# Optimization experiments

Hardware: AMD Instinct MI355X
Metric: run time of the kernel (lower is better)

## Reference

```python
import jax, jax.numpy as jnp
import numpy as np

N, D = 50000, 1000
FH1, FH2 = 256, 128
GH1, GH2, H = 64, 30, 3
NC = 10
E = 800000
BN_EPS = 1e-5


def setup_inputs() -> dict:
    key = jax.random.key(0)
    ks = iter(jax.random.split(key, 48))
    nk = lambda: next(ks)
    r = lambda *s: jax.random.normal(nk(), s, jnp.float32) * 0.05
    g = lambda n: 1.0 + jax.random.normal(nk(), (n,), jnp.float32) * 0.01
    return dict(
        x=jax.random.normal(nk(), (N, D), jnp.float32),
        edge_index=jax.random.randint(nk(), (2, E), 0, N, dtype=jnp.int32),
        enc_w1=r(D, FH1), enc_b1=r(FH1), enc_g1=g(FH1), enc_bt1=r(FH1),
        enc_w2=r(FH1, FH2), enc_b2=r(FH2), enc_g2=g(FH2), enc_bt2=r(FH2),
        gat1_w=r(FH2, H * GH1), gat1_asrc=r(H, GH1), gat1_adst=r(H, GH1), gat1_b=r(H * GH1),
        gat2_w=r(H * GH1, GH2), gat2_asrc=r(1, GH2), gat2_adst=r(1, GH2), gat2_b=r(GH2),
        gat3_w=r(H * GH1, GH2), gat3_asrc=r(1, GH2), gat3_adst=r(1, GH2), gat3_b=r(GH2),
        dec_w1=r(GH2, FH2), dec_b1=r(FH2), dec_g1=g(FH2), dec_bt1=r(FH2),
        dec_w2=r(FH2, FH1), dec_b2=r(FH1), dec_g2=g(FH1), dec_bt2=r(FH1),
        dec_w3=r(FH1, D), dec_b3=r(D),
        clu_w1=r(GH2, FH2), clu_b1=r(FH2), clu_g1=g(FH2), clu_bt1=r(FH2),
        clu_w2=r(FH2, NC), clu_b2=r(NC),
    )


def _bn_elu(h, w, b, gm, bt):
    # Linear -> BatchNorm1d (batch stats) -> ELU; dropout is identity at eval
    h = h @ w + b
    m = h.mean(0)
    v = h.var(0)
    return jax.nn.elu(gm * (h - m) * jax.lax.rsqrt(v + BN_EPS) + bt)


def _gat(h, src, dst, n, w, a_src, a_dst, b, heads, oc, concat):
    # PyG GATConv: per-head linear, edge-wise LeakyReLU(0.2) scores,
    # softmax over incoming edges of each dst node, weighted scatter-sum.
    hh = (h @ w).reshape(n, heads, oc)            # [N,H,C]
    s_src = jnp.sum(hh * a_src, -1)               # [N,H]
    s_dst = jnp.sum(hh * a_dst, -1)               # [N,H]
    e = jax.nn.leaky_relu(s_src[src] + s_dst[dst], negative_slope=0.2)  # [E,H]
    m = jax.ops.segment_max(e, dst, num_segments=n)
    p = jnp.exp(e - m[dst])
    denom = jax.ops.segment_sum(p, dst, num_segments=n)
    alpha = p / denom[dst]                        # [E,H]
    msg = hh[src] * alpha[..., None]              # [E,H,C]
    out = jax.ops.segment_sum(msg, dst, num_segments=n)
    out = out.reshape(n, heads * oc) if concat else out.mean(1)
    return out + b


def reference(x, edge_index,
              enc_w1, enc_b1, enc_g1, enc_bt1, enc_w2, enc_b2, enc_g2, enc_bt2,
              gat1_w, gat1_asrc, gat1_adst, gat1_b,
              gat2_w, gat2_asrc, gat2_adst, gat2_b,
              gat3_w, gat3_asrc, gat3_adst, gat3_b,
              dec_w1, dec_b1, dec_g1, dec_bt1, dec_w2, dec_b2, dec_g2, dec_bt2, dec_w3, dec_b3,
              clu_w1, clu_b1, clu_g1, clu_bt1, clu_w2, clu_b2):
    n = x.shape[0]
    loops = jnp.arange(n, dtype=edge_index.dtype)  # GATConv add_self_loops=True
    src = jnp.concatenate([edge_index[0], loops])
    dst = jnp.concatenate([edge_index[1], loops])

    h = _bn_elu(x, enc_w1, enc_b1, enc_g1, enc_bt1)
    h = _bn_elu(h, enc_w2, enc_b2, enc_g2, enc_bt2)
    h = jax.nn.relu(_gat(h, src, dst, n, gat1_w, gat1_asrc, gat1_adst, gat1_b, H, GH1, True))
    mu = _gat(h, src, dst, n, gat2_w, gat2_asrc, gat2_adst, gat2_b, 1, GH2, False)
    logvar = _gat(h, src, dst, n, gat3_w, gat3_asrc, gat3_adst, gat3_b, 1, GH2, False)
    z = mu  # eval-mode reparameterize returns mu

    d = _bn_elu(z, dec_w1, dec_b1, dec_g1, dec_bt1)
    d = _bn_elu(d, dec_w2, dec_b2, dec_g2, dec_bt2)
    x_rec = d @ dec_w3 + dec_b3

    c = _bn_elu(z, clu_w1, clu_b1, clu_g1, clu_bt1)
    pred = jax.nn.softmax(c @ clu_w2 + clu_b2, axis=1)
    return (pred, x_rec, z, mu, logvar)
```

## Files before the change

kernel.cpp:

```cpp
#include <hip/hip_runtime.h>
#include <hip/hip_bf16.h>

typedef short short8 __attribute__((ext_vector_type(8)));
typedef short short4v __attribute__((ext_vector_type(4)));
typedef float f32x4 __attribute__((ext_vector_type(4)));

static __device__ __forceinline__ short f2bf(float f){
  __hip_bfloat16 h = __float2bfloat16(f);
  return __builtin_bit_cast(short, h);
}
static __device__ __forceinline__ float b2f(short s){
  unsigned int u = ((unsigned int)(unsigned short)s) << 16;
  return __builtin_bit_cast(float, u);
}
static __device__ __forceinline__ float lrelu(float x){ return x > 0.f ? x : 0.2f*x; }
static __device__ __forceinline__ float eluf(float x){ return x > 0.f ? x : (__expf(x)-1.f); }
static __device__ __forceinline__ int imin(int a,int b){ return a<b?a:b; }

typedef const __attribute__((address_space(1))) void as1_void;
typedef __attribute__((address_space(3))) void as3_void;
static __device__ __forceinline__ void gload16(const void* g, void* l){
  __builtin_amdgcn_global_load_lds((as1_void*)g, (as3_void*)l, 16, 0, 0);
}
template<int NN> __device__ __forceinline__ void wait_vm(){
  if constexpr (NN==0) asm volatile("s_waitcnt vmcnt(0)" ::: "memory");
  else if constexpr (NN==3) asm volatile("s_waitcnt vmcnt(3)" ::: "memory");
  else if constexpr (NN==4) asm volatile("s_waitcnt vmcnt(4)" ::: "memory");
  else if constexpr (NN==6) asm volatile("s_waitcnt vmcnt(6)" ::: "memory");
  else if constexpr (NN==8) asm volatile("s_waitcnt vmcnt(8)" ::: "memory");
  else asm volatile("s_waitcnt vmcnt(0)" ::: "memory");
}

template<int BN, bool OBF16, bool CST, bool SMAX, bool G23S, bool G1S>
static __device__ __forceinline__ void gemm_core(int wg, short* lds,
    const short* __restrict__ A, int lda, const short* __restrict__ Bt, int ldb,
    void* __restrict__ Cv, int ldc, const float* __restrict__ bias,
    int M, int N, int K, int nbn,
    float* __restrict__ o_sum, float* __restrict__ o_sq,
    float* __restrict__ s2s, float* __restrict__ s2d,
    float* __restrict__ s3s, float* __restrict__ s3d,
    const float* __restrict__ a2s, const float* __restrict__ a2d,
    const float* __restrict__ a3s, const float* __restrict__ a3d)
{
  constexpr int BM = 128, BK = 32, GPR = 4;
  constexpr int WM = BM/2, WN = BN/2;
  constexpr int FM = WM/16, FN = WN/16;
  constexpr int AI = (BM*GPR)/(4*64);
  constexpr int BI_T = (BN*GPR)/64;
  constexpr bool BDUP = (BI_T < 4);
  constexpr int BI = BDUP ? BI_T : BI_T/4;
  constexpr int LPT = AI + BI;
  constexpr int TS = (BM+BN)*BK;

  const int tid = threadIdx.x, wid = tid>>6, lane = tid&63;
  const int wm = wid>>1, wn = wid&1;
  int bmt = wg / nbn, bnt = wg - bmt*nbn;
  const int bm = bmt*BM, bn = bnt*BN;
  const int lr = lane&15, lg = lane>>4;
  const int nt = (K + BK - 1)/BK;

  f32x4 acc[FM][FN] = {};

  auto STAGE = [&](int t){
    int buf = t % 3, k0 = t*BK;
    #pragma unroll
    for (int i=0;i<AI;i++){
      int ci = wid*AI + i;
      int c = ci*64 + lane;
      int row = c>>2, g = c&3;
      int gr = imin(bm+row, M-1);
      const short* src = A + (size_t)gr*lda + k0 + ((g ^ (row&3))<<3);
      gload16(src, &lds[buf*TS + ci*512]);
    }
    #pragma unroll
    for (int i=0;i<BI;i++){
      int bi = BDUP ? i : wid*BI + i;
      int c = bi*64 + lane;
      int row = c>>2, g = c&3;
      const short* src = Bt + (size_t)(bn+row)*ldb + k0 + ((g ^ (row&3))<<3);
      gload16(src, &lds[buf*TS + BM*BK + bi*512]);
    }
  };

  for (int s=0; s<2 && s<nt; ++s) STAGE(s);

  for (int t=0; t<nt; ++t){
    int newer = imin(nt, t+2) - t - 1;
    if (newer >= 1) wait_vm<LPT>();
    else wait_vm<0>();
    __builtin_amdgcn_s_barrier();
    __builtin_amdgcn_sched_barrier(0);
    if (t+2 < nt) STAGE(t+2);
    int buf = t % 3;
    short8 af[FM], bf[FN];
    #pragma unroll
    for (int m=0;m<FM;m++){
      int r = wm*WM + m*16 + lr;
      af[m] = *(short8*)&lds[buf*TS + r*BK + ((lg ^ (r&3))<<3)];
    }
    #pragma unroll
    for (int n=0;n<FN;n++){
      int r = wn*WN + n*16 + lr;
      bf[n] = *(short8*)&lds[buf*TS + BM*BK + r*BK + ((lg ^ (r&3))<<3)];
    }
    #pragma unroll
    for (int m=0;m<FM;m++)
      #pragma unroll
      for (int n=0;n<FN;n++)
        acc[m][n] = __builtin_amdgcn_mfma_f32_16x16x32_bf16(af[m], bf[n], acc[m][n], 0, 0, 0);
  }

  if (SMAX){
    #pragma unroll
    for (int m=0;m<FM;m++)
      #pragma unroll
      for (int q=0;q<4;q++){
        int row = bm + wm*WM + m*16 + lg*4 + q;
        float v = (lr < 10) ? (acc[m][0][q] + bias[lr]) : -3e38f;
        float mx = v;
        #pragma unroll
        for (int d=1; d<16; d<<=1) mx = fmaxf(mx, __shfl_xor(mx, d));
        float e = (lr < 10) ? __expf(v - mx) : 0.f;
        float sm = e;
        #pragma unroll
        for (int d=1; d<16; d<<=1) sm += __shfl_xor(sm, d);
        if (wn == 0 && lr < 10 && row < M)
          ((float*)Cv)[(size_t)row*10 + lr] = e/sm;
      }
    return;
  }

  #pragma unroll
  for (int m=0;m<FM;m++)
    #pragma unroll
    for (int n=0;n<FN;n++)
      #pragma unroll
      for (int q=0;q<4;q++){
        int row = bm + wm*WM + m*16 + lg*4 + q;
        int col = bn + wn*WN + n*16 + lr;
        if (row < M && col < N){
          float v = acc[m][n][q];
          if (bias) v += bias[col];
          if (OBF16) ((short*)Cv)[(size_t)row*ldc + col] = f2bf(v);
          else       ((float*)Cv)[(size_t)row*ldc + col] = v;
        }
      }

  if (G1S){
    int h = bnt;
    float a_s[FN], a_d[FN];
    #pragma unroll
    for (int n=0;n<FN;n++){
      int cl = wn*WN + n*16 + lr;
      a_s[n] = a2s[h*64 + cl];
      a_d[n] = a2d[h*64 + cl];
    }
    #pragma unroll
    for (int m=0;m<FM;m++)
      #pragma unroll
      for (int q=0;q<4;q++){
        int row = bm + wm*WM + m*16 + lg*4 + q;
        float ps = 0.f, pd = 0.f;
        #pragma unroll
        for (int n=0;n<FN;n++){ ps += acc[m][n][q]*a_s[n]; pd += acc[m][n][q]*a_d[n]; }
        #pragma unroll
        for (int d=1; d<16; d<<=1){ ps += __shfl_xor(ps, d); pd += __shfl_xor(pd, d); }
        if (lr == 0 && row < M){
          atomicAdd(&s2s[row*3+h], ps);
          atomicAdd(&s2d[row*3+h], pd);
        }
      }
  }

  if (G23S){
    float a_s[FN], a_d[FN];
    #pragma unroll
    for (int n=0;n<FN;n++){
      int cl = n*16 + lr;
      bool valid = cl < 30;
      a_s[n] = valid ? (wn ? a3s[cl] : a2s[cl]) : 0.f;
      a_d[n] = valid ? (wn ? a3d[cl] : a2d[cl]) : 0.f;
    }
    #pragma unroll
    for (int m=0;m<FM;m++)
      #pragma unroll
      for (int q=0;q<4;q++){
        int row = bm + wm*WM + m*16 + lg*4 + q;
        float ps = 0.f, pd = 0.f;
        #pragma unroll
        for (int n=0;n<FN;n++){ ps += acc[m][n][q]*a_s[n]; pd += acc[m][n][q]*a_d[n]; }
        #pragma unroll
        for (int d=1; d<16; d<<=1){ ps += __shfl_xor(ps, d); pd += __shfl_xor(pd, d); }
        if (lr == 0 && row < M){
          if (wn){ s3s[row] = ps; s3d[row] = pd; }
          else   { s2s[row] = ps; s2d[row] = pd; }
        }
      }
  }

  if (CST){
    #pragma unroll
    for (int n=0;n<FN;n++){
      float s = 0.f, q2 = 0.f;
      #pragma unroll
      for (int m=0;m<FM;m++)
        #pragma unroll
        for (int q=0;q<4;q++){
          int row = bm + wm*WM + m*16 + lg*4 + q;
          if (row < M){ float v = acc[m][n][q]; s += v; q2 += v*v; }
        }
      s  += __shfl_xor(s, 16);  s += __shfl_xor(s, 32);
      q2 += __shfl_xor(q2, 16); q2 += __shfl_xor(q2, 32);
      if (lg == 0){
        int col = bn + wn*WN + n*16 + lr;
        if (col < N){ atomicAdd(&o_sum[col], s); atomicAdd(&o_sq[col], q2); }
      }
    }
  }
}

static __device__ __forceinline__ int xcd_swz(int bid, int nwg){
  int q8 = nwg >> 3, r8 = nwg & 7;
  int xcd = bid & 7, pos = bid >> 3;
  return (xcd < r8 ? xcd*(q8+1) : r8*(q8+1) + (xcd-r8)*q8) + pos;
}

template<int BN, bool OBF16, bool CST, bool SMAX, bool G23S, bool G1S>
__global__ __launch_bounds__(256) void gemm_g(
    const short* __restrict__ A, int lda, const short* __restrict__ Bt, int ldb,
    void* __restrict__ Cv, int ldc, const float* __restrict__ bias,
    int M, int N, int K, int nbn,
    float* __restrict__ o_sum, float* __restrict__ o_sq,
    float* __restrict__ s2s, float* __restrict__ s2d,
    float* __restrict__ s3s, float* __restrict__ s3d,
    const float* __restrict__ a2s, const float* __restrict__ a2d,
    const float* __restrict__ a3s, const float* __restrict__ a3d)
{
  __shared__ short lds[3*(128+BN)*32];
  int wg = xcd_swz(blockIdx.x, gridDim.x);
  gemm_core<BN,OBF16,CST,SMAX,G23S,G1S>(wg, lds, A, lda, Bt, ldb, Cv, ldc, bias,
      M, N, K, nbn, o_sum, o_sq, s2s, s2d, s3s, s3d, a2s, a2d, a3s, a3d);
}

__global__ __launch_bounds__(256) void gemm_dual(
    const short* __restrict__ A1, int lda1, const short* __restrict__ B1, int ldb1,
    void* __restrict__ C1, int ldc1, const float* __restrict__ bias1, int N1, int K1,
    const short* __restrict__ A2, int lda2, const short* __restrict__ B2, int ldb2,
    void* __restrict__ C2, const float* __restrict__ bias2, int N2, int K2,
    int M, int split)
{
  __shared__ short lds[3*(128+128)*32];
  int wg = xcd_swz(blockIdx.x, gridDim.x);
  if (wg < split){
    gemm_core<128,false,false,false,false,false>(wg, lds, A1, lda1, B1, ldb1, C1, ldc1, bias1,
        M, N1, K1, 8, nullptr,nullptr, nullptr,nullptr,nullptr,nullptr, nullptr,nullptr,nullptr,nullptr);
  } else {
    gemm_core<32,false,false,true,false,false>(wg - split, lds, A2, lda2, B2, ldb2, C2, 10, bias2,
        M, N2, K2, 1, nullptr,nullptr, nullptr,nullptr,nullptr,nullptr, nullptr,nullptr,nullptr,nullptr);
  }
}

__global__ __launch_bounds__(256) void cvt_hist(const float* __restrict__ x, short* __restrict__ xb, int M,
                                                int CB, const int* __restrict__ d, int E, int* __restrict__ deg){
  int b = blockIdx.x;
  if (b < CB){
    int row = b*2 + (threadIdx.x>>7);
    int c8  = (threadIdx.x&127)*8;
    if (row >= M || c8 >= 1000) return;
    const float* p = x + (size_t)row*1000 + c8;
    float4 f0 = *(const float4*)p, f1 = *(const float4*)(p+4);
    short8 o;
    o[0]=f2bf(f0.x);o[1]=f2bf(f0.y);o[2]=f2bf(f0.z);o[3]=f2bf(f0.w);
    o[4]=f2bf(f1.x);o[5]=f2bf(f1.y);o[6]=f2bf(f1.z);o[7]=f2bf(f1.w);
    *(short8*)&xb[(size_t)row*1000 + c8] = o;
  } else {
    int i = (b - CB)*256 + threadIdx.x;
    if (i < E) atomicAdd(&deg[d[i]], 1);
  }
}

struct WEnt { const float* src; short* dst; int K, N, KP, NR; };
struct WTab { WEnt e[10]; };
__global__ __launch_bounds__(256) void wtrans_all(WTab tab){
  WEnt w = tab.e[blockIdx.y];
  int gid = blockIdx.x*256 + threadIdx.x;
  if (gid >= w.NR * w.KP) return;
  int n = gid / w.KP, k = gid - n*w.KP;
  float v = (k < w.K && n < w.N) ? w.src[(size_t)k*w.N + n] : 0.f;
  w.dst[gid] = f2bf(v);
}

template<int C>
__global__ __launch_bounds__(256) void bn_elu_apply2(const short* __restrict__ H, short* __restrict__ O,
    int M, float invM,
    const float* __restrict__ ssum, const float* __restrict__ ssq,
    const float* __restrict__ g, const float* __restrict__ bt){
  __shared__ float sc[C], sh[C];
  for (int c = threadIdx.x; c < C; c += 256){
    float mn  = ssum[c]*invM;
    float var = ssq[c]*invM - mn*mn;
    float s = g[c]*rsqrtf(var + 1e-5f);
    sc[c] = s; sh[c] = bt[c] - mn*s;
  }
  __syncthreads();
  int total8 = M*(C/8);
  for (int i = blockIdx.x*256+threadIdx.x; i < total8; i += gridDim.x*256){
    short8 v = ((const short8*)H)[i];
    int cb = (i*8) & (C-1);
    short8 o;
    #pragma unroll
    for (int j=0;j<8;j++) o[j] = f2bf(eluf(b2f(v[j])*sc[cb+j]+sh[cb+j]));
    ((short8*)O)[i] = o;
  }
}

__global__ __launch_bounds__(256) void bn_elu_split(const short* __restrict__ H,
    short* __restrict__ Od, short* __restrict__ Oc, int M, float invM,
    const float* __restrict__ ssum, const float* __restrict__ ssq,
    const float* __restrict__ gd, const float* __restrict__ btd,
    const float* __restrict__ gc, const float* __restrict__ btc){
  __shared__ float sc[256], sh[256];
  {
    int c = threadIdx.x;
    float mn  = ssum[c]*invM;
    float var = ssq[c]*invM - mn*mn;
    float gg = (c<128) ? gd[c] : gc[c-128];
    float bb = (c<128) ? btd[c] : btc[c-128];
    float s = gg*rsqrtf(var + 1e-5f);
    sc[c] = s; sh[c] = bb - mn*s;
  }
  __syncthreads();
  int total8 = M*32;
  for (int i = blockIdx.x*256+threadIdx.x; i < total8; i += gridDim.x*256){
    short8 v = ((const short8*)H)[i];
    int cb = (i*8) & 255;
    short8 o;
    #pragma unroll
    for (int j=0;j<8;j++) o[j] = f2bf(eluf(b2f(v[j])*sc[cb+j]+sh[cb+j]));
    int row = i>>5;
    short* O = (cb < 128) ? Od : Oc;
    *(short8*)&O[(size_t)row*128 + (cb&127)] = o;
  }
}

__global__ __launch_bounds__(256) void scan1(const int* __restrict__ deg, int* __restrict__ offs,
                                             int* __restrict__ bsum, int n){
  __shared__ int sm[256];
  int tid = threadIdx.x;
  int base = blockIdx.x*1024 + tid*4;
  int v0 = base+0<n ? deg[base+0] : 0;
  int v1 = base+1<n ? deg[base+1] : 0;
  int v2 = base+2<n ? deg[base+2] : 0;
  int v3 = base+3<n ? deg[base+3] : 0;
  int ts = v0+v1+v2+v3;
  sm[tid] = ts;
  __syncthreads();
  #pragma unroll
  for (int d=1; d<256; d<<=1){
    int t = (tid>=d) ? sm[tid-d] : 0;
    __syncthreads();
    sm[tid] += t;
    __syncthreads();
  }
  int ex = sm[tid] - ts;
  if (base+0<n) offs[base+0] = ex;
  if (base+1<n) offs[base+1] = ex+v0;
  if (base+2<n) offs[base+2] = ex+v0+v1;
  if (base+3<n) offs[base+3] = ex+v0+v1+v2;
  if (tid==255) bsum[blockIdx.x] = sm[255];
}
__global__ __launch_bounds__(256) void scan3(int* __restrict__ offs, const int* __restrict__ bsum,
                      int* __restrict__ cursor, int n, int total){
  __shared__ int base_sm;
  int tgt = blockIdx.x >> 2;
  if (threadIdx.x < 64){
    int j = threadIdx.x;
    int v = (j < tgt) ? bsum[j] : 0;
    #pragma unroll
    for (int d=32; d; d>>=1) v += __shfl_xor(v, d);
    if (j == 0) base_sm = v;
  }
  __syncthreads();
  int i = blockIdx.x*256 + threadIdx.x;
  if (i < n){ int v = offs[i] + base_sm; offs[i]=v; cursor[i]=v; }
  if (i == 0) offs[n] = total;
}
__global__ void scatter_kernel(const int* __restrict__ s, const int* __restrict__ d, int E,
                               int* __restrict__ cursor, int* __restrict__ csr){
  int i = blockIdx.x*256 + threadIdx.x;
  if (i < E){ int pos = atomicAdd(&cursor[d[i]], 1); csr[pos] = s[i]; }
}

__global__ __launch_bounds__(256) void gat1_gather_bf(const int* __restrict__ offs, const int* __restrict__ csr,
    const short* __restrict__ hh, const float* __restrict__ ss, const float* __restrict__ sd,
    const float* __restrict__ bias, short* __restrict__ out, int n){
  int w = threadIdx.x >> 6, lane = threadIdx.x & 63;
  int dst = blockIdx.x*4 + w;
  if (dst >= n) return;
  float sd0 = sd[dst*3+0], sd1 = sd[dst*3+1], sd2 = sd[dst*3+2];
  float p0 = __expf(lrelu(ss[dst*3+0]+sd0));
  float p1 = __expf(lrelu(ss[dst*3+1]+sd1));
  float p2 = __expf(lrelu(ss[dst*3+2]+sd2));
  const short* hr = hh + (size_t)dst*192;
  float a0 = p0*b2f(hr[lane]), a1 = p1*b2f(hr[64+lane]), a2 = p2*b2f(hr[128+lane]);
  float d0 = p0, d1 = p1, d2 = p2;
  int p = offs[dst], pe = offs[dst+1];
  int n0=0,n1=0,n2=0,n3=0;
  if (p+4 <= pe){ n0=csr[p]; n1=csr[p+1]; n2=csr[p+2]; n3=csr[p+3]; }
  while (p+4 <= pe){
    int s0=n0, s1=n1, s2=n2, s3=n3;
    int pn = p+4;
    if (pn+4 <= pe){ n0=csr[pn]; n1=csr[pn+1]; n2=csr[pn+2]; n3=csr[pn+3]; }
    float e00=ss[s0*3+0], e01=ss[s0*3+1], e02=ss[s0*3+2];
    float e10=ss[s1*3+0], e11=ss[s1*3+1], e12=ss[s1*3+2];
    float e20=ss[s2*3+0], e21=ss[s2*3+1], e22=ss[s2*3+2];
    float e30=ss[s3*3+0], e31=ss[s3*3+1], e32=ss[s3*3+2];
    const short* r0 = hh + (size_t)s0*192;
    const short* r1 = hh + (size_t)s1*192;
    const short* r2 = hh + (size_t)s2*192;
    const short* r3 = hh + (size_t)s3*192;
    float v00=b2f(r0[lane]), v01=b2f(r0[64+lane]), v02=b2f(r0[128+lane]);
    float v10=b2f(r1[lane]), v11=b2f(r1[64+lane]), v12=b2f(r1[128+lane]);
    float v20=b2f(r2[lane]), v21=b2f(r2[64+lane]), v22=b2f(r2[128+lane]);
    float v30=b2f(r3[lane]), v31=b2f(r3[64+lane]), v32=b2f(r3[128+lane]);
    float q00=__expf(lrelu(e00+sd0)), q01=__expf(lrelu(e01+sd1)), q02=__expf(lrelu(e02+sd2));
    float q10=__expf(lrelu(e10+sd0)), q11=__expf(lrelu(e11+sd1)), q12=__expf(lrelu(e12+sd2));
    float q20=__expf(lrelu(e20+sd0)), q21=__expf(lrelu(e21+sd1)), q22=__expf(lrelu(e22+sd2));
    float q30=__expf(lrelu(e30+sd0)), q31=__expf(lrelu(e31+sd1)), q32=__expf(lrelu(e32+sd2));
    a0 += q00*v00 + q10*v10 + q20*v20 + q30*v30;
    a1 += q01*v01 + q11*v11 + q21*v21 + q31*v31;
    a2 += q02*v02 + q12*v12 + q22*v22 + q32*v32;
    d0 += q00+q10+q20+q30;
    d1 += q01+q11+q21+q31;
    d2 += q02+q12+q22+q32;
    p = pn;
  }
  for (; p < pe; ++p){
    int src = csr[p];
    float q0 = __expf(lrelu(ss[src*3+0]+sd0));
    float q1 = __expf(lrelu(ss[src*3+1]+sd1));
    float q2 = __expf(lrelu(ss[src*3+2]+sd2));
    const short* sr = hh + (size_t)src*192;
    a0 += q0*b2f(sr[lane]); a1 += q1*b2f(sr[64+lane]); a2 += q2*b2f(sr[128+lane]);
    d0 += q0; d1 += q1; d2 += q2;
  }
  float v0 = a0/d0 + bias[lane];
  float v1 = a1/d1 + bias[64+lane];
  float v2 = a2/d2 + bias[128+lane];
  short* orow = out + (size_t)dst*192;
  orow[lane]      = f2bf(v0 > 0.f ? v0 : 0.f);
  orow[64+lane]   = f2bf(v1 > 0.f ? v1 : 0.f);
  orow[128+lane]  = f2bf(v2 > 0.f ? v2 : 0.f);
}

__global__ __launch_bounds__(256) void gat23_gather(const int* __restrict__ offs, const int* __restrict__ csr,
    const short* __restrict__ hh23,
    const float* __restrict__ s2s, const float* __restrict__ s2d,
    const float* __restrict__ s3s, const float* __restrict__ s3d,
    const float* __restrict__ b2, const float* __restrict__ b3,
    float* __restrict__ zs, float* __restrict__ mus, float* __restrict__ lvs,
    short* __restrict__ zbf, int n){
  int w = threadIdx.x >> 6, lane = threadIdx.x & 63;
  int dst = blockIdx.x*4 + w;
  if (dst >= n) return;
  bool lo = lane < 32;
  int c = lane & 31;
  bool valid = c < 30;
  float sdA = s2d[dst], sdB = s3d[dst];
  float sdx = lo ? sdA : sdB;
  const float* ssx = lo ? s2s : s3s;
  float p2 = __expf(lrelu(s2s[dst]+sdA));
  float p3 = __expf(lrelu(s3s[dst]+sdB));
  float val = valid ? b2f(hh23[(size_t)dst*64+lane]) : 0.f;
  float acc = (lo ? p2 : p3) * val;
  float den2 = p2, den3 = p3;
  int p = offs[dst], pe = offs[dst+1];
  int n0=0,n1=0,n2=0,n3=0;
  if (p+4 <= pe){ n0=csr[p]; n1=csr[p+1]; n2=csr[p+2]; n3=csr[p+3]; }
  while (p+4 <= pe){
    int s0=n0, s1=n1, s2i=n2, s3i=n3;
    int pn = p+4;
    if (pn+4 <= pe){ n0=csr[pn]; n1=csr[pn+1]; n2=csr[pn+2]; n3=csr[pn+3]; }
    float eA0=ssx[s0], eA1=ssx[s1], eA2=ssx[s2i], eA3=ssx[s3i];
    float f20=s2s[s0], f21=s2s[s1], f22=s2s[s2i], f23=s2s[s3i];
    float f30=s3s[s0], f31=s3s[s1], f32=s3s[s2i], f33=s3s[s3i];
    float v0 = valid ? b2f(hh23[(size_t)s0*64+lane]) : 0.f;
    float v1 = valid ? b2f(hh23[(size_t)s1*64+lane]) : 0.f;
    float v2 = valid ? b2f(hh23[(size_t)s2i*64+lane]) : 0.f;
    float v3 = valid ? b2f(hh23[(size_t)s3i*64+lane]) : 0.f;
    float qx0=__expf(lrelu(eA0+sdx)), qx1=__expf(lrelu(eA1+sdx));
    float qx2=__expf(lrelu(eA2+sdx)), qx3=__expf(lrelu(eA3+sdx));
    acc += qx0*v0 + qx1*v1 + qx2*v2 + qx3*v3;
    den2 += __expf(lrelu(f20+sdA)) + __expf(lrelu(f21+sdA)) + __expf(lrelu(f22+sdA)) + __expf(lrelu(f23+sdA));
    den3 += __expf(lrelu(f30+sdB)) + __expf(lrelu(f31+sdB)) + __expf(lrelu(f32+sdB)) + __expf(lrelu(f33+sdB));
    p = pn;
  }
  for (; p < pe; ++p){
    int src = csr[p];
    float q2 = __expf(lrelu(s2s[src]+sdA));
    float q3 = __expf(lrelu(s3s[src]+sdB));
    float v = valid ? b2f(hh23[(size_t)src*64+lane]) : 0.f;
    acc += (lo ? q2 : q3) * v;
    den2 += q2; den3 += q3;
  }
  if (lo){
    if (valid){
      float v = acc/den2 + b2[c];
      zs[(size_t)dst*30+c]  = v;
      mus[(size_t)dst*30+c] = v;
      zbf[(size_t)dst*32+c] = f2bf(v);
    } else {
      zbf[(size_t)dst*32+c] = 0;
    }
  } else if (valid){
    lvs[(size_t)dst*30+c] = acc/den3 + b3[c];
  }
}

static inline int cdiv(int a, int b){ return (a + b - 1) / b; }

extern "C" void kernel_launch(void* const* d_in, const int* in_sizes, int n_in,
                              void* d_out, int out_size, void* d_ws, size_t ws_size,
                              hipStream_t stream)
{
  const float* x        = (const float*)d_in[0];
  const int*   ei       = (const int*)  d_in[1];
  const float* enc_w1   = (const float*)d_in[2];
  const float* enc_g1   = (const float*)d_in[4];
  const float* enc_bt1  = (const float*)d_in[5];
  const float* enc_w2   = (const float*)d_in[6];
  const float* enc_g2   = (const float*)d_in[8];
  const float* enc_bt2  = (const float*)d_in[9];
  const float* gat1_w   = (const float*)d_in[10];
  const float* gat1_as  = (const float*)d_in[11];
  const float* gat1_ad  = (const float*)d_in[12];
  const float* gat1_b   = (const float*)d_in[13];
  const float* gat2_w   = (const float*)d_in[14];
  const float* gat2_as  = (const float*)d_in[15];
  const float* gat2_ad  = (const float*)d_in[16];
  const float* gat2_b   = (const float*)d_in[17];
  const float* gat3_w   = (const float*)d_in[18];
  const float* gat3_as  = (const float*)d_in[19];
  const float* gat3_ad  = (const float*)d_in[20];
  const float* gat3_b   = (const float*)d_in[21];
  const float* dec_w1   = (const float*)d_in[22];
  const float* dec_g1   = (const float*)d_in[24];
  const float* dec_bt1  = (const float*)d_in[25];
  const float* dec_w2   = (const float*)d_in[26];
  const float* dec_g2   = (const float*)d_in[28];
  const float* dec_bt2  = (const float*)d_in[29];
  const float* dec_w3   = (const float*)d_in[30];
  const float* dec_b3   = (const float*)d_in[31];
  const float* clu_w1   = (const float*)d_in[32];
  const float* clu_g1   = (const float*)d_in[34];
  const float* clu_bt1  = (const float*)d_in[35];
  const float* clu_w2   = (const float*)d_in[36];
  const float* clu_b2   = (const float*)d_in[37];

  const int N = in_sizes[0] / 1000;
  const int E = in_sizes[1] / 2;
  const int* e_src = ei;
  const int* e_dst = ei + E;
  const float invN = 1.f/(float)N;

  float* out  = (float*)d_out;
  float* pred = out;
  float* xrec = out + (size_t)N*10;
  float* zs   = xrec + (size_t)N*1000;
  float* mus  = zs  + (size_t)N*30;
  float* lvs  = mus + (size_t)N*30;

  char* ws = (char*)d_ws;
  size_t off = 0;
  auto alloc = [&](size_t bytes)->char*{
    char* p = ws + off;
    off = (off + bytes + 255) & ~(size_t)255;
    return p;
  };
  short* t_enc1  = (short*)alloc(256*1024*2);
  short* t_enc2  = (short*)alloc(128*256*2);
  short* t_gat1  = (short*)alloc(256*128*2);
  short* t_gat23 = (short*)alloc(64*192*2);
  short* t_dc1   = (short*)alloc(256*32*2);
  short* t_dec2  = (short*)alloc(256*128*2);
  short* t_dec3  = (short*)alloc(1024*256*2);
  short* t_clu2  = (short*)alloc(32*128*2);
  float* h1f  = (float*)alloc((size_t)N*256*4);
  short* h1b  = (short*)alloc((size_t)N*256*2);
  float* h2f  = (float*)alloc((size_t)N*128*4);
  short* h2b  = (short*)alloc((size_t)N*128*2);
  short* hh1b = (short*)alloc((size_t)N*192*2);
  short* h3b  = (short*)alloc((size_t)N*192*2);
  float* hh23f= (float*)alloc((size_t)N*64*4);
  short* zbf  = (short*)alloc((size_t)N*32*2);
  size_t zcnt = 2048 + (size_t)6*N + (N+1);
  float* stats= (float*)alloc(zcnt*4);
  float* ss1  = stats + 2048;
  float* sd1  = ss1 + (size_t)3*N;
  int*   deg  = (int*)(sd1 + (size_t)3*N);
  float* s2s  = (float*)alloc((size_t)N*4);
  float* s2d  = (float*)alloc((size_t)N*4);
  float* s3s  = (float*)alloc((size_t)N*4);
  float* s3d  = (float*)alloc((size_t)N*4);
  int*   offs = (int*)alloc((size_t)(N+1)*4);
  int*   curp = (int*)alloc((size_t)(N+1)*4);
  int*   bsum = (int*)alloc(256*4);
  int*   csr  = (int*)alloc((size_t)E*4);
  short* xb     = h1b;
  short* h1pre  = (short*)h1f;
  short* h2pre  = (short*)h2f;
  short* hh23b  = (short*)hh23f;
  short* dc1pre = (short*)h2f;
  short* d1b    = h3b;
  short* c1b    = hh1b;
  short* d2pre  = (short*)h1f;
  short* d2b    = h1b;
  float* st_enc1 = stats, *st_enc2 = stats+512, *st_dc1 = stats+768, *st_dec2 = stats+1280;

  WTab tab;
  tab.e[0]  = {enc_w1, t_enc1, 1000, 256, 1024, 256};
  tab.e[1]  = {enc_w2, t_enc2, 256, 128, 256, 128};
  tab.e[2]  = {gat1_w, t_gat1, 128, 192, 128, 256};
  tab.e[3]  = {gat2_w, t_gat23, 192, 30, 192, 32};
  tab.e[4]  = {gat3_w, t_gat23 + 32*192, 192, 30, 192, 32};
  tab.e[5]  = {dec_w1, t_dc1, 30, 128, 32, 128};
  tab.e[6]  = {clu_w1, t_dc1 + 128*32, 30, 128, 32, 128};
  tab.e[7]  = {dec_w2, t_dec2, 128, 256, 128, 256};
  tab.e[8]  = {dec_w3, t_dec3, 256, 1000, 256, 1024};
  tab.e[9]  = {clu_w2, t_clu2, 128, 10, 128, 32};
  wtrans_all<<<dim3(1024, 10), 256, 0, stream>>>(tab);
  hipMemsetAsync(stats, 0, zcnt*4, stream);

  int CB = cdiv(N, 2);
  cvt_hist<<<CB + cdiv(E,256), 256, 0, stream>>>(x, xb, N, CB, e_dst, E, deg);

  int nb = cdiv(N, 1024);
  scan1<<<nb, 256, 0, stream>>>(deg, offs, bsum, N);
  scan3<<<cdiv(N,256), 256, 0, stream>>>(offs, bsum, curp, N, E);
  scatter_kernel<<<cdiv(E,256), 256, 0, stream>>>(e_src, e_dst, E, curp, csr);

  const int MB = cdiv(N, 128);

  gemm_g<128,true,true,false,false,false><<<MB*2, 256, 0, stream>>>(
      xb, 1000, t_enc1, 1024, h1pre, 256, nullptr, N, 256, 1000, 2,
      st_enc1, st_enc1+256, nullptr,nullptr,nullptr,nullptr, nullptr,nullptr,nullptr,nullptr);
  bn_elu_apply2<256><<<2048, 256, 0, stream>>>(h1pre, h1b, N, invN, st_enc1, st_enc1+256, enc_g1, enc_bt1);

  gemm_g<128,true,true,false,false,false><<<MB, 256, 0, stream>>>(
      h1b, 256, t_enc2, 256, h2pre, 128, nullptr, N, 128, 256, 1,
      st_enc2, st_enc2+128, nullptr,nullptr,nullptr,nullptr, nullptr,nullptr,nullptr,nullptr);
  bn_elu_apply2<128><<<2048, 256, 0, stream>>>(h2pre, h2b, N, invN, st_enc2, st_enc2+128, enc_g2, enc_bt2);

  gemm_g<64,true,false,false,false,true><<<MB*3, 256, 0, stream>>>(
      h2b, 128, t_gat1, 128, hh1b, 192, nullptr, N, 192, 128, 3,
      nullptr,nullptr, ss1,sd1,nullptr,nullptr, gat1_as,gat1_ad,nullptr,nullptr);
  gat1_gather_bf<<<cdiv(N,4), 256, 0, stream>>>(offs, csr, hh1b, ss1, sd1, gat1_b, h3b, N);

  gemm_g<64,true,false,false,true,false><<<MB, 256, 0, stream>>>(
      h3b, 192, t_gat23, 192, hh23b, 64, nullptr, N, 64, 192, 1,
      nullptr,nullptr, s2s,s2d,s3s,s3d, gat2_as,gat2_ad,gat3_as,gat3_ad);
  gat23_gather<<<cdiv(N,4), 256, 0, stream>>>(offs, csr, hh23b, s2s, s2d, s3s, s3d, gat2_b, gat3_b, zs, mus, lvs, zbf, N);

  gemm_g<128,true,true,false,false,false><<<MB*2, 256, 0, stream>>>(
      zbf, 32, t_dc1, 32, dc1pre, 256, nullptr, N, 256, 32, 2,
      st_dc1, st_dc1+256, nullptr,nullptr,nullptr,nullptr, nullptr,nullptr,nullptr,nullptr);
  bn_elu_split<<<2048, 256, 0, stream>>>(dc1pre, d1b, c1b, N, invN, st_dc1, st_dc1+256, dec_g1, dec_bt1, clu_g1, clu_bt1);

  gemm_g<128,true,true,false,false,false><<<MB*2, 256, 0, stream>>>(
      d1b, 128, t_dec2, 128, d2pre, 256, nullptr, N, 256, 128, 2,
      st_dec2, st_dec2+256, nullptr,nullptr,nullptr,nullptr, nullptr,nullptr,nullptr,nullptr);
  bn_elu_apply2<256><<<2048, 256, 0, stream>>>(d2pre, d2b, N, invN, st_dec2, st_dec2+256, dec_g2, dec_bt2);

  gemm_dual<<<MB*8 + MB, 256, 0, stream>>>(
      d2b, 256, t_dec3, 256, xrec, 1000, dec_b3, 1000, 256,
      c1b, 128, t_clu2, 128, pred, clu_b2, 10, 128,
      N, MB*8);
}
```

Baseline: 616.0 us.

## Fuse fp32-to-bf16 input conversion into the first encoder GEMM

```diff
diff --git a/kernel.cpp b/kernel.cpp
--- a/kernel.cpp
+++ b/kernel.cpp
@@ -29,6 +29,12 @@
   else if constexpr (NN==6) asm volatile("s_waitcnt vmcnt(6)" ::: "memory");
   else if constexpr (NN==8) asm volatile("s_waitcnt vmcnt(8)" ::: "memory");
   else asm volatile("s_waitcnt vmcnt(0)" ::: "memory");
+}
+
+static __device__ __forceinline__ int xcd_swz(int bid, int nwg){
+  int q8 = nwg >> 3, r8 = nwg & 7;
+  int xcd = bid & 7, pos = bid >> 3;
+  return (xcd < r8 ? xcd*(q8+1) : r8*(q8+1) + (xcd-r8)*q8) + pos;
 }
 
 template<int BN, bool OBF16, bool CST, bool SMAX, bool G23S, bool G1S>
@@ -219,12 +225,6 @@
   }
 }
 
-static __device__ __forceinline__ int xcd_swz(int bid, int nwg){
-  int q8 = nwg >> 3, r8 = nwg & 7;
-  int xcd = bid & 7, pos = bid >> 3;
-  return (xcd < r8 ? xcd*(q8+1) : r8*(q8+1) + (xcd-r8)*q8) + pos;
-}
-
 template<int BN, bool OBF16, bool CST, bool SMAX, bool G23S, bool G1S>
 __global__ __launch_bounds__(256) void gemm_g(
     const short* __restrict__ A, int lda, const short* __restrict__ Bt, int ldb,
@@ -260,23 +260,109 @@
   }
 }
 
-__global__ __launch_bounds__(256) void cvt_hist(const float* __restrict__ x, short* __restrict__ xb, int M,
-                                                int CB, const int* __restrict__ d, int E, int* __restrict__ deg){
-  int b = blockIdx.x;
-  if (b < CB){
-    int row = b*2 + (threadIdx.x>>7);
-    int c8  = (threadIdx.x&127)*8;
-    if (row >= M || c8 >= 1000) return;
-    const float* p = x + (size_t)row*1000 + c8;
-    float4 f0 = *(const float4*)p, f1 = *(const float4*)(p+4);
-    short8 o;
-    o[0]=f2bf(f0.x);o[1]=f2bf(f0.y);o[2]=f2bf(f0.z);o[3]=f2bf(f0.w);
-    o[4]=f2bf(f1.x);o[5]=f2bf(f1.y);o[6]=f2bf(f1.z);o[7]=f2bf(f1.w);
-    *(short8*)&xb[(size_t)row*1000 + c8] = o;
-  } else {
-    int i = (b - CB)*256 + threadIdx.x;
-    if (i < E) atomicAdd(&deg[d[i]], 1);
-  }
+__global__ __launch_bounds__(256) void gemm_f32a(
+    const float* __restrict__ A, int lda, const short* __restrict__ Bt, int ldb,
+    short* __restrict__ C, int ldc,
+    int M, int N, int K, int nbn,
+    float* __restrict__ o_sum, float* __restrict__ o_sq)
+{
+  constexpr int BM=128, BN=128, BK=32;
+  constexpr int ATS = BM*64;
+  constexpr int TSH = ATS + BN*32;
+  __shared__ short lds[3*TSH];
+  const int tid=threadIdx.x, wid=tid>>6, lane=tid&63;
+  const int wm=wid>>1, wn=wid&1;
+  int wg = xcd_swz(blockIdx.x, gridDim.x);
+  int bmt = wg/nbn, bnt = wg - bmt*nbn;
+  const int bm=bmt*BM, bn=bnt*BN;
+  const int lr=lane&15, lg=lane>>4;
+  const int nt=(K+BK-1)/BK;
+  f32x4 acc[4][4]={};
+
+  auto STAGE=[&](int t){
+    int buf=t%3, k0=t*BK;
+    #pragma unroll
+    for (int i=0;i<4;i++){
+      int ci = wid*4+i;
+      int c = ci*64+lane;
+      int row=c>>3, g=c&7;
+      int gr=imin(bm+row, M-1);
+      const float* src = A + (size_t)gr*lda + k0 + ((g ^ (row&7))<<2);
+      gload16(src, &lds[buf*TSH + ci*512]);
+    }
+    #pragma unroll
+    for (int i=0;i<2;i++){
+      int bi = wid*2+i;
+      int c = bi*64+lane;
+      int row=c>>2, g=c&3;
+      const short* src = Bt + (size_t)(bn+row)*ldb + k0 + ((g ^ (row&3))<<3);
+      gload16(src, &lds[buf*TSH + ATS + bi*512]);
+    }
+  };
+
+  STAGE(0); if (nt>1) STAGE(1);
+  for (int t=0;t<nt;++t){
+    int newer = imin(nt,t+2)-t-1;
+    if (newer>=1) wait_vm<6>(); else wait_vm<0>();
+    __builtin_amdgcn_s_barrier();
+    __builtin_amdgcn_sched_barrier(0);
+    if (t+2<nt) STAGE(t+2);
+    int buf=t%3;
+    short8 af[4], bf[4];
+    #pragma unroll
+    for (int m=0;m<4;m++){
+      int r = wm*64 + m*16 + lr;
+      int g0 = (2*lg) ^ (r&7), g1 = (2*lg+1) ^ (r&7);
+      float4 fa = *(float4*)&lds[buf*TSH + r*64 + g0*8];
+      float4 fb = *(float4*)&lds[buf*TSH + r*64 + g1*8];
+      af[m][0]=f2bf(fa.x); af[m][1]=f2bf(fa.y); af[m][2]=f2bf(fa.z); af[m][3]=f2bf(fa.w);
+      af[m][4]=f2bf(fb.x); af[m][5]=f2bf(fb.y); af[m][6]=f2bf(fb.z); af[m][7]=f2bf(fb.w);
+    }
+    #pragma unroll
+    for (int n=0;n<4;n++){
+      int r = wn*64 + n*16 + lr;
+      bf[n] = *(short8*)&lds[buf*TSH + ATS + r*32 + ((lg ^ (r&3))<<3)];
+    }
+    #pragma unroll
+    for (int m=0;m<4;m++)
+      #pragma unroll
+      for (int n=0;n<4;n++)
+        acc[m][n] = __builtin_amdgcn_mfma_f32_16x16x32_bf16(af[m], bf[n], acc[m][n], 0, 0, 0);
+  }
+
+  #pragma unroll
+  for (int m=0;m<4;m++)
+    #pragma unroll
+    for (int n=0;n<4;n++)
+      #pragma unroll
+      for (int q=0;q<4;q++){
+        int row = bm + wm*64 + m*16 + lg*4 + q;
+        int col = bn + wn*64 + n*16 + lr;
+        if (row < M && col < N)
+          C[(size_t)row*ldc + col] = f2bf(acc[m][n][q]);
+      }
+  #pragma unroll
+  for (int n=0;n<4;n++){
+    float s = 0.f, q2 = 0.f;
+    #pragma unroll
+    for (int m=0;m<4;m++)
+      #pragma unroll
+      for (int q=0;q<4;q++){
+        int row = bm + wm*64 + m*16 + lg*4 + q;
+        if (row < M){ float v = acc[m][n][q]; s += v; q2 += v*v; }
+      }
+    s  += __shfl_xor(s, 16);  s += __shfl_xor(s, 32);
+    q2 += __shfl_xor(q2, 16); q2 += __shfl_xor(q2, 32);
+    if (lg == 0){
+      int col = bn + wn*64 + n*16 + lr;
+      if (col < N){ atomicAdd(&o_sum[col], s); atomicAdd(&o_sq[col], q2); }
+    }
+  }
+}
+
+__global__ void hist_kernel(const int* __restrict__ d, int E, int* __restrict__ deg){
+  int i = blockIdx.x*256 + threadIdx.x;
+  if (i < E) atomicAdd(&deg[d[i]], 1);
 }
 
 struct WEnt { const float* src; short* dst; int K, N, KP, NR; };
@@ -606,7 +692,6 @@
   int*   curp = (int*)alloc((size_t)(N+1)*4);
   int*   bsum = (int*)alloc(256*4);
   int*   csr  = (int*)alloc((size_t)E*4);
-  short* xb     = h1b;
   short* h1pre  = (short*)h1f;
   short* h2pre  = (short*)h2f;
   short* hh23b  = (short*)hh23f;
@@ -631,9 +716,7 @@
   wtrans_all<<<dim3(1024, 10), 256, 0, stream>>>(tab);
   hipMemsetAsync(stats, 0, zcnt*4, stream);
 
-  int CB = cdiv(N, 2);
-  cvt_hist<<<CB + cdiv(E,256), 256, 0, stream>>>(x, xb, N, CB, e_dst, E, deg);
-
+  hist_kernel<<<cdiv(E,256), 256, 0, stream>>>(e_dst, E, deg);
   int nb = cdiv(N, 1024);
   scan1<<<nb, 256, 0, stream>>>(deg, offs, bsum, N);
   scan3<<<cdiv(N,256), 256, 0, stream>>>(offs, bsum, curp, N, E);
@@ -641,9 +724,8 @@
 
   const int MB = cdiv(N, 128);
 
-  gemm_g<128,true,true,false,false,false><<<MB*2, 256, 0, stream>>>(
-      xb, 1000, t_enc1, 1024, h1pre, 256, nullptr, N, 256, 1000, 2,
-      st_enc1, st_enc1+256, nullptr,nullptr,nullptr,nullptr, nullptr,nullptr,nullptr,nullptr);
+  gemm_f32a<<<MB*2, 256, 0, stream>>>(
+      x, 1000, t_enc1, 1024, h1pre, 256, N, 256, 1000, 2, st_enc1, st_enc1+256);
   bn_elu_apply2<256><<<2048, 256, 0, stream>>>(h1pre, h1b, N, invN, st_enc1, st_enc1+256, enc_g1, enc_bt1);
 
   gemm_g<128,true,true,false,false,false><<<MB, 256, 0, stream>>>(
```

After: 601.8 us. 1.02x faster.
